# Kernel tuning notes

Hardware: AMD Instinct MI355X
Metric: run time of the kernel (lower is better)

The kernel has to match this reference:

```python
import jax, jax.numpy as jnp
import numpy as np
from jax import lax

# ---- module constants (mirror CorrelatedSphericalField.__init__) ----
NLAT = 361
NLON = 2 * NLAT
LMAX = NLAT            # number of degrees l
MMAX = NLAT + 1        # number of orders m = nlon//2 + 1
N_LATENT = 16
T_STEPS = 8
LENGTH_SCALE = 500_000.0
TIME_SCALE = 48.0
SIGMA = 0.3
DT = 6.0
R_EARTH = 6_371_000.0
PHI = float(np.exp(-DT / TIME_SCALE))
KT = (LENGTH_SCALE / R_EARTH) ** 2 / 2.0
FOUR_PI = float(4.0 * np.pi)


def _precompute_pct():
    """Associated Legendre tensor pct[m, l, k] for InverseRealSHT,
    equiangular grid, norm='backward' (orthonormal P / sqrt(4pi)), with
    Condon-Shortley phase -- matches torch_harmonics _precompute_legpoly(inverse=True)."""
    theta = np.linspace(0.0, np.pi, NLAT)      # equiangular incl. poles
    x = np.cos(theta)
    s = np.sin(theta)
    nmax = max(MMAX, LMAX)
    vdm = np.zeros((nmax, nmax, NLAT), dtype=np.float64)  # [m, l, lat]
    vdm[0, 0] = 1.0 / np.sqrt(4.0 * np.pi)
    for m in range(1, nmax):                    # diagonal P_m^m
        vdm[m, m] = np.sqrt((2.0 * m + 1.0) / (2.0 * m)) * s * vdm[m - 1, m - 1]
    for m in range(nmax - 1):                   # P_{m+1}^m
        vdm[m, m + 1] = np.sqrt(2.0 * m + 3.0) * x * vdm[m, m]
    for l in range(2, nmax):                    # three-term recurrence, vectorized over m
        ms = np.arange(l - 1)
        a = np.sqrt((4.0 * l * l - 1.0) / (l * l - ms * ms))[:, None]
        b = np.sqrt(((l - 1.0) ** 2 - ms * ms) / (4.0 * (l - 1.0) ** 2 - 1.0))[:, None]
        vdm[ms, l] = a * (x[None, :] * vdm[ms, l - 1] - b * vdm[ms, l - 2])
    vdm[1::2] *= -1.0                           # Condon-Shortley phase
    pct = vdm[:MMAX, :LMAX] / np.sqrt(4.0 * np.pi)  # norm='backward', inverse=True
    return jnp.asarray(pct, dtype=jnp.float32)


def _make_sigma_n():
    j = np.arange(1, NLAT, dtype=np.float64)
    denom = 2.0 * np.sum((2.0 * j + 1.0) * np.exp(-KT * j * (j + 1.0)))
    F0 = np.sqrt(SIGMA ** 2 * (1.0 - PHI ** 2) / denom)
    l = np.arange(NLAT, dtype=np.float64)
    prods = np.repeat((l * (l + 1.0))[:, None], MMAX, axis=1)   # (nlat, nlat+1)
    sn = np.tril(np.exp(-KT * prods / 2.0) * F0)                # keep m <= l
    return jnp.asarray(sn, dtype=jnp.float32)


def setup_inputs() -> dict:
    key = jax.random.key(0)
    k0, k1 = jax.random.split(key)
    sigma_n = _make_sigma_n()
    # initial stationary AR(1) coefficients: (1-phi^2)^{-1/2} * sigma_n * xi0
    xi0 = jax.random.normal(k0, (N_LATENT, LMAX, MMAX, 2), dtype=jnp.float32)
    coeff0 = (1.0 - PHI ** 2) ** (-0.5) * sigma_n[None, :, :, None] * xi0
    # pre-drawn innovations for the T AR(1) updates (real/imag stacked)
    xi = jax.random.normal(k1, (T_STEPS, N_LATENT, LMAX, MMAX, 2), dtype=jnp.float32)
    pct = _precompute_pct()
    x = jnp.zeros((T_STEPS,), dtype=jnp.int32)   # only x.shape[0] is used
    return {"x": x, "sigma_n": sigma_n, "coeff0": coeff0, "xi": xi, "pct": pct}


def reference(x, sigma_n, coeff0, xi, pct):
    T = x.shape[0]
    c0 = coeff0[..., 0] + 1j * coeff0[..., 1]    # (N, L, M) complex64
    xic = xi[..., 0] + 1j * xi[..., 1]           # (T, N, L, M) complex64

    # AR(1): emit coeff BEFORE update (matches the torch loop ordering)
    def step(c, xk):
        return PHI * c + sigma_n * xk, c

    _, coeffs = lax.scan(step, c0, xic[:T])      # (T, N, L, M)

    # inverse real SHT, batched over all T steps at once:
    # xs[..., k, m] = sum_l coeff[..., l, m] * pct[m, l, k]
    re = jnp.einsum('tnlm,mlk->tnkm', coeffs.real, pct)
    im = jnp.einsum('tnlm,mlk->tnkm', coeffs.imag, pct)
    xs = re + 1j * im                            # (T, N, nlat, mmax)
    out = jnp.fft.irfft(xs, n=NLON, axis=-1, norm='forward') * FOUR_PI
    return out.reshape(T, 1, 1, N_LATENT, NLAT, NLON)
```

## Files before the change

kernel.cpp:

```cpp
#include <hip/hip_runtime.h>
#include <math.h>

#define NLATC   361
#define NLONC   722
#define MMAXC   362
#define LMAXC   361
#define NLK     16
#define TSTEPS  8
#define LCUT    128
#define MCUT    128
#define MCK     256
#define TNK     46208
#define NPAD    768
#define KPAD    384
#define PHI_F   0.8824969025845955f
#define FOURPI  12.566370614359172f
#define ASCALE  1024.0f
#define OSCALE  0.0009765625f

typedef _Float16 half8 __attribute__((ext_vector_type(8)));
typedef float floatx4 __attribute__((ext_vector_type(4)));

__global__ __launch_bounds__(256) void k_prep(const float* __restrict__ sigma_n,
                                              const float* __restrict__ coeff0,
                                              const float* __restrict__ xi,
                                              const float* __restrict__ pct,
                                              _Float16* __restrict__ Bf,
                                              _Float16* __restrict__ pTf,
                                              _Float16* __restrict__ cB) {
    __shared__ _Float16 sm[64][66];
    int bid = blockIdx.x;
    int tid = threadIdx.x;

    if (bid < 768) {
        int idx = bid * 256 + tid;
        int j = idx >> 8, mc = idx & 255;
        int m = mc >> 1, c = mc & 1;
        float v = 0.0f;
        if (j < NLONC) {
            int r = (m * j) % NLONC;
            float th = (float)r * (6.283185307179586f / 722.0f);
            float s, co;
            sincosf(th, &s, &co);
            float wq = (m == 0 ? 1.0f : 2.0f) * FOURPI;
            v = c ? (-wq * s) : (wq * co);
        }
        Bf[idx] = (_Float16)v;
    } else if (bid < 2304) {
        int b = bid - 768;
        int k0 = (b % 6) * 64;
        int l0 = ((b / 6) & 1) * 64;
        int m  = b / 12;
        int tx = tid & 63, ty = tid >> 6;
#pragma unroll
        for (int i = 0; i < 16; ++i) {
            int row = ty * 16 + i;
            int k = k0 + tx;
            sm[row][tx] = (k < NLATC)
                ? (_Float16)pct[((size_t)m * LMAXC + l0 + row) * NLATC + k] : (_Float16)0.0f;
        }
        __syncthreads();
#pragma unroll
        for (int i = 0; i < 16; ++i) {
            int kr = ty * 16 + i;
            pTf[((size_t)m * KPAD + k0 + kr) * 128 + l0 + tx] = sm[tx][kr];
        }
    } else {
        int b = bid - 2304;
        int mt = b & 3, lt = (b >> 2) & 1, n = b >> 3;
        int ml = tid & 31, lg = tid >> 5;
        int m  = mt * 32 + ml;
        int l0 = lt * 64 + lg * 8;
        float cr[8], ci[8], sg[8];
#pragma unroll
        for (int i = 0; i < 8; ++i) {
            int l = l0 + i;
            sg[i] = sigma_n[(size_t)l * MMAXC + m];
            float2 c0 = *(const float2*)&coeff0[(((size_t)n * LMAXC + l) * MMAXC + m) * 2];
            cr[i] = c0.x; ci[i] = c0.y;
        }
#pragma unroll
        for (int t = 0; t < TSTEPS; ++t) {
            half8 hr, hi;
#pragma unroll
            for (int i = 0; i < 8; ++i) {
                hr[i] = (_Float16)(cr[i] * ASCALE);
                hi[i] = (_Float16)(ci[i] * ASCALE);
            }
            size_t rowR = ((size_t)m * 256 +       t * 16 + n) * 128 + l0;
            size_t rowI = ((size_t)m * 256 + 128 + t * 16 + n) * 128 + l0;
            *(half8*)&cB[rowR] = hr;
            *(half8*)&cB[rowI] = hi;
            if (t < TSTEPS - 1) {
#pragma unroll
                for (int i = 0; i < 8; ++i) {
                    float2 x = *(const float2*)
                        &xi[((((size_t)t * NLK + n) * LMAXC + l0 + i) * MMAXC + m) * 2];
                    cr[i] = PHI_F * cr[i] + sg[i] * x.x;
                    ci[i] = PHI_F * ci[i] + sg[i] * x.y;
                }
            }
        }
    }
}

__global__ __launch_bounds__(256) void k_leg(const _Float16* __restrict__ cB,
                                             const _Float16* __restrict__ pTf,
                                             _Float16* __restrict__ xsTh) {
    __shared__ _Float16 As[256][40];
    __shared__ _Float16 Bs[64][40];
    int tid = threadIdx.x;
    int k0c = blockIdx.x * 64;
    int m   = blockIdx.y;
    int w = tid >> 6, lane = tid & 63, m16 = lane & 15, quad = lane >> 4;
    floatx4 acc[4][4];
#pragma unroll
    for (int i = 0; i < 4; ++i)
#pragma unroll
        for (int j = 0; j < 4; ++j) acc[i][j] = (floatx4)(0.0f);

    int lt0 = m & ~31;
    for (int lt = lt0; lt < 128; lt += 32) {
#pragma unroll
        for (int it = 0; it < 4; ++it) {
            int r = (tid >> 2) + 64 * it, lc = (tid & 3) * 8;
            *(half8*)&As[r][lc] = *(const half8*)&cB[((size_t)m * 256 + r) * 128 + lt + lc];
        }
        {
            int k = tid >> 2, lc = (tid & 3) * 8;
            *(half8*)&Bs[k][lc] = *(const half8*)&pTf[((size_t)m * KPAD + k0c + k) * 128 + lt + lc];
        }
        __syncthreads();
        half8 a[4], b[4];
#pragma unroll
        for (int i = 0; i < 4; ++i) a[i] = *(const half8*)&As[w * 64 + i * 16 + m16][quad * 8];
#pragma unroll
        for (int j = 0; j < 4; ++j) b[j] = *(const half8*)&Bs[j * 16 + m16][quad * 8];
#pragma unroll
        for (int i = 0; i < 4; ++i)
#pragma unroll
            for (int j = 0; j < 4; ++j)
                acc[i][j] = __builtin_amdgcn_mfma_f32_16x16x32_f16(a[i], b[j], acc[i][j], 0, 0, 0);
        __syncthreads();
    }
#pragma unroll
    for (int i = 0; i < 4; ++i)
#pragma unroll
        for (int j = 0; j < 4; ++j)
#pragma unroll
            for (int reg = 0; reg < 4; ++reg) {
                int r = w * 64 + i * 16 + quad * 4 + reg;
                int c = r >> 7, tn = r & 127;
                int k = k0c + j * 16 + m16;
                if (k < NLATC)
                    xsTh[(size_t)(2 * m + c) * TNK + tn * NLATC + k] = (_Float16)acc[i][j][reg];
            }
}

__global__ __launch_bounds__(256) void k_castXs(const _Float16* __restrict__ xsTh,
                                                _Float16* __restrict__ xsA) {
    __shared__ _Float16 sm[64][66];
    int tx = threadIdx.x & 63, ty = threadIdx.x >> 6;
    int t0  = blockIdx.x * 64;
    int mc0 = blockIdx.y * 64;
#pragma unroll
    for (int i = 0; i < 16; ++i) {
        int row = ty * 16 + i;
        sm[row][tx] = xsTh[(size_t)(mc0 + row) * TNK + t0 + tx];
    }
    __syncthreads();
#pragma unroll
    for (int i = 0; i < 16; ++i) {
        int row = ty * 16 + i;
        xsA[(size_t)(t0 + row) * MCK + mc0 + tx] = sm[tx][row];
    }
}

__global__ __launch_bounds__(256) void k_gemm2(const _Float16* __restrict__ A,
                                               const _Float16* __restrict__ Bf,
                                               float* __restrict__ C) {
    __shared__ _Float16 As[128][40];
    __shared__ _Float16 Bs[128][40];
    int tid = threadIdx.x;
    int row0 = blockIdx.x * 128;
    int j0   = blockIdx.y * 128;
    int w = tid >> 6, lane = tid & 63, m16 = lane & 15, quad = lane >> 4;
    int wr = (w & 1) * 64, wc = (w >> 1) * 64;
    floatx4 acc[4][4];
#pragma unroll
    for (int i = 0; i < 4; ++i)
#pragma unroll
        for (int j = 0; j < 4; ++j) acc[i][j] = (floatx4)(0.0f);

    for (int k0 = 0; k0 < MCK; k0 += 32) {
#pragma unroll
        for (int it = 0; it < 2; ++it) {
            int r = (tid >> 2) + 64 * it, kc = (tid & 3) * 8;
            *(half8*)&As[r][kc] = *(const half8*)&A[(size_t)(row0 + r) * MCK + k0 + kc];
            *(half8*)&Bs[r][kc] = *(const half8*)&Bf[(size_t)(j0 + r) * MCK + k0 + kc];
        }
        __syncthreads();
        half8 a[4], b[4];
#pragma unroll
        for (int i = 0; i < 4; ++i) a[i] = *(const half8*)&As[wr + i * 16 + m16][quad * 8];
#pragma unroll
        for (int j = 0; j < 4; ++j) b[j] = *(const half8*)&Bs[wc + j * 16 + m16][quad * 8];
#pragma unroll
        for (int i = 0; i < 4; ++i)
#pragma unroll
            for (int j = 0; j < 4; ++j)
                acc[i][j] = __builtin_amdgcn_mfma_f32_16x16x32_f16(a[i], b[j], acc[i][j], 0, 0, 0);
        __syncthreads();
    }
#pragma unroll
    for (int i = 0; i < 4; ++i)
#pragma unroll
        for (int j = 0; j < 4; ++j)
#pragma unroll
            for (int reg = 0; reg < 4; ++reg) {
                int row = row0 + wr + i * 16 + quad * 4 + reg;
                int col = j0 + wc + j * 16 + m16;
                if (col < NLONC)
                    C[(size_t)row * NLONC + col] = acc[i][j][reg] * OSCALE;
            }
}

extern "C" void kernel_launch(void* const* d_in, const int* in_sizes, int n_in,
                              void* d_out, int out_size, void* d_ws, size_t ws_size,
                              hipStream_t stream) {
    (void)in_sizes; (void)n_in; (void)out_size; (void)ws_size;
    const float* sigma_n = (const float*)d_in[1];
    const float* coeff0  = (const float*)d_in[2];
    const float* xi      = (const float*)d_in[3];
    const float* pct     = (const float*)d_in[4];
    float* out = (float*)d_out;

    char* ws = (char*)d_ws;
    size_t off = 0;
    _Float16* cB   = (_Float16*)(ws + off); off += (size_t)128 * 256 * 128 * 2;
    _Float16* pTf  = (_Float16*)(ws + off); off += (size_t)128 * KPAD * 128 * 2;
    _Float16* xsTh = (_Float16*)(ws + off); off += (size_t)MCK * TNK * 2;
    _Float16* xsA  = (_Float16*)(ws + off); off += (size_t)TNK * MCK * 2;
    _Float16* Bf   = (_Float16*)(ws + off); off += (size_t)NPAD * MCK * 2;

    k_prep<<<2432, 256, 0, stream>>>(sigma_n, coeff0, xi, pct, Bf, pTf, cB);
    k_leg<<<dim3(6, 128), 256, 0, stream>>>(cB, pTf, xsTh);
    k_castXs<<<dim3(722, 4), 256, 0, stream>>>(xsTh, xsA);
    k_gemm2<<<dim3(361, 6), 256, 0, stream>>>(xsA, Bf, out);
}
```

Before: 414.4 us.

## Use direct global-to-LDS loads in GEMMs and remap gemm2 blocks per XCD

Replaces the register-staged global loads into shared memory in k_leg and k_gemm2 with the global_load_lds builtin, which writes 16 bytes per lane straight into LDS. The shared arrays drop their padding so the wave-contiguous layout matches what the builtin writes. k_gemm2's grid is also transposed and remapped so consecutive tiles land on the same XCD, aiming at better L2 reuse of the B operand and A rows. Removing the padding may bring back LDS bank conflicts on the MFMA fragment reads, and the remap depends on the XCD round-robin dispatch order.

```diff
diff --git a/kernel.cpp b/kernel.cpp
--- a/kernel.cpp
+++ b/kernel.cpp
@@ -21,6 +21,10 @@
 typedef _Float16 half8 __attribute__((ext_vector_type(8)));
 typedef float floatx4 __attribute__((ext_vector_type(4)));
 
+#define GLOAD16(g, l) __builtin_amdgcn_global_load_lds( \
+    (const __attribute__((address_space(1))) void*)(g), \
+    (__attribute__((address_space(3))) void*)(l), 16, 0, 0)
+
 __global__ __launch_bounds__(256) void k_prep(const float* __restrict__ sigma_n,
                                               const float* __restrict__ coeff0,
                                               const float* __restrict__ xi,
@@ -107,12 +111,14 @@
 __global__ __launch_bounds__(256) void k_leg(const _Float16* __restrict__ cB,
                                              const _Float16* __restrict__ pTf,
                                              _Float16* __restrict__ xsTh) {
-    __shared__ _Float16 As[256][40];
-    __shared__ _Float16 Bs[64][40];
+    __shared__ _Float16 As[256][32];
+    __shared__ _Float16 Bs[64][32];
     int tid = threadIdx.x;
     int k0c = blockIdx.x * 64;
     int m   = blockIdx.y;
     int w = tid >> 6, lane = tid & 63, m16 = lane & 15, quad = lane >> 4;
+    int rA = lane >> 2;
+    int cA = (lane & 3) * 8;
     floatx4 acc[4][4];
 #pragma unroll
     for (int i = 0; i < 4; ++i)
@@ -122,13 +128,13 @@
     int lt0 = m & ~31;
     for (int lt = lt0; lt < 128; lt += 32) {
 #pragma unroll
-        for (int it = 0; it < 4; ++it) {
-            int r = (tid >> 2) + 64 * it, lc = (tid & 3) * 8;
-            *(half8*)&As[r][lc] = *(const half8*)&cB[((size_t)m * 256 + r) * 128 + lt + lc];
+        for (int c = 0; c < 4; ++c) {
+            int rr = w * 64 + c * 16;
+            GLOAD16(&cB[((size_t)m * 256 + rr + rA) * 128 + lt + cA], &As[rr][0]);
         }
         {
-            int k = tid >> 2, lc = (tid & 3) * 8;
-            *(half8*)&Bs[k][lc] = *(const half8*)&pTf[((size_t)m * KPAD + k0c + k) * 128 + lt + lc];
+            int rr = w * 16;
+            GLOAD16(&pTf[((size_t)m * KPAD + k0c + rr + rA) * 128 + lt + cA], &Bs[rr][0]);
         }
         __syncthreads();
         half8 a[4], b[4];
@@ -179,13 +185,17 @@
 __global__ __launch_bounds__(256) void k_gemm2(const _Float16* __restrict__ A,
                                                const _Float16* __restrict__ Bf,
                                                float* __restrict__ C) {
-    __shared__ _Float16 As[128][40];
-    __shared__ _Float16 Bs[128][40];
+    __shared__ _Float16 As[128][32];
+    __shared__ _Float16 Bs[128][32];
     int tid = threadIdx.x;
-    int row0 = blockIdx.x * 128;
-    int j0   = blockIdx.y * 128;
     int w = tid >> 6, lane = tid & 63, m16 = lane & 15, quad = lane >> 4;
+    int lin = blockIdx.y * 6 + blockIdx.x;
+    int xcd = lin & 7, idx = lin >> 3;
+    int wg  = (xcd < 6) ? xcd * 271 + idx : 1626 + (xcd - 6) * 270 + idx;
+    int row0 = (wg / 6) * 128;
+    int j0   = (wg % 6) * 128;
     int wr = (w & 1) * 64, wc = (w >> 1) * 64;
+    int rA = lane >> 2, cA = (lane & 3) * 8;
     floatx4 acc[4][4];
 #pragma unroll
     for (int i = 0; i < 4; ++i)
@@ -194,10 +204,10 @@
 
     for (int k0 = 0; k0 < MCK; k0 += 32) {
 #pragma unroll
-        for (int it = 0; it < 2; ++it) {
-            int r = (tid >> 2) + 64 * it, kc = (tid & 3) * 8;
-            *(half8*)&As[r][kc] = *(const half8*)&A[(size_t)(row0 + r) * MCK + k0 + kc];
-            *(half8*)&Bs[r][kc] = *(const half8*)&Bf[(size_t)(j0 + r) * MCK + k0 + kc];
+        for (int c = 0; c < 2; ++c) {
+            int rr = w * 32 + c * 16;
+            GLOAD16(&A [(size_t)(row0 + rr + rA) * MCK + k0 + cA], &As[rr][0]);
+            GLOAD16(&Bf[(size_t)(j0   + rr + rA) * MCK + k0 + cA], &Bs[rr][0]);
         }
         __syncthreads();
         half8 a[4], b[4];
@@ -246,5 +256,5 @@
     k_prep<<<2432, 256, 0, stream>>>(sigma_n, coeff0, xi, pct, Bf, pTf, cB);
     k_leg<<<dim3(6, 128), 256, 0, stream>>>(cB, pTf, xsTh);
     k_castXs<<<dim3(722, 4), 256, 0, stream>>>(xsTh, xsA);
-    k_gemm2<<<dim3(361, 6), 256, 0, stream>>>(xsA, Bf, out);
-}
+    k_gemm2<<<dim3(6, 361), 256, 0, stream>>>(xsA, Bf, out);
+}
```

New measurement: 389.7 us. -6.0%, faster.
